# Kernel optimization log

Hardware: AMD Instinct MI355X
Metric: run time of the kernel (lower is better)

The kernel has to match this reference:

```python
import jax, jax.numpy as jnp
import numpy as np

N_NODES = 100000
N_EDGES = 6400000
NODE_IN = 128
HID = 64


def _mlp(x, w1, b1, w2, b2):
    # Linear -> ReLU -> Linear -> ReLU
    return jax.nn.relu(jax.nn.relu(x @ w1 + b1) @ w2 + b2)


def _edge_softmax_agg(node_h, logits, src, dst, n):
    # DGL edge_softmax: softmax of edge logits over incoming edges per dst node,
    # then weighted sum of src node features scattered to dst.
    m = jax.lax.stop_gradient(jax.ops.segment_max(logits, dst, num_segments=n))
    e = jnp.exp(logits - m[dst])
    s = jax.ops.segment_sum(e, dst, num_segments=n)
    w = e / s[dst]
    return jax.ops.segment_sum(w * node_h[src], dst, num_segments=n)


def setup_inputs() -> dict:
    key = jax.random.key(0)
    ks = jax.random.split(key, 24)
    d = {
        "node_feat": jax.random.normal(ks[0], (N_NODES, NODE_IN), jnp.float32),
        "edge_feat": jax.random.normal(ks[1], (N_EDGES, 1), jnp.float32),
        "edge_dist": jax.random.normal(ks[2], (N_EDGES, 1), jnp.float32),
        "src": jax.random.randint(ks[3], (N_EDGES,), 0, N_NODES, jnp.int32),
        "dst": jax.random.randint(ks[4], (N_EDGES,), 0, N_NODES, jnp.int32),
    }
    def lin(k, fin, fout):
        kw, kb = jax.random.split(k)
        return (jax.random.normal(kw, (fin, fout), jnp.float32) / np.sqrt(fin),
                jax.random.normal(kb, (fout,), jnp.float32) * 0.01)
    d["enc_w1"], d["enc_b1"] = lin(ks[5], NODE_IN, HID)
    d["enc_w2"], d["enc_b2"] = lin(ks[6], HID, 1)
    d["nu_w1"], d["nu_b1"] = lin(ks[7], 2, HID)
    d["nu_w2"], d["nu_b2"] = lin(ks[8], HID, 1)
    d["eu_w1"], d["eu_b1"] = lin(ks[9], 3, HID)
    d["eu_w2"], d["eu_b2"] = lin(ks[10], HID, 1)
    d["dec_w1"], d["dec_b1"] = lin(ks[11], 1, HID)
    d["dec_w2"], d["dec_b2"] = lin(ks[12], HID, 1)
    return d


def reference(node_feat, edge_feat, edge_dist, src, dst,
              enc_w1, enc_b1, enc_w2, enc_b2,
              nu_w1, nu_b1, nu_w2, nu_b2,
              eu_w1, eu_b1, eu_w2, eu_b2,
              dec_w1, dec_b1, dec_w2, dec_b2):
    n = node_feat.shape[0]
    # encoder on raw node features -> [N,1]
    h = _mlp(node_feat, enc_w1, enc_b1, enc_w2, enc_b2)
    # softmax aggregation weighted by edge 'dist'
    h = _edge_softmax_agg(h, edge_dist, src, dst, n)
    # edge update: concat([edge_feat, src_h, dst_h]) -> MLP -> [E,1]
    eh = _mlp(jnp.concatenate([edge_feat, h[src], h[dst]], axis=-1),
              eu_w1, eu_b1, eu_w2, eu_b2)
    # pull: sum incoming updated edge features per dst node
    agg = jax.ops.segment_sum(eh, dst, num_segments=n)
    # node update: concat([agg_m, h]) -> MLP -> [N,1]
    h = _mlp(jnp.concatenate([agg, h], axis=-1), nu_w1, nu_b1, nu_w2, nu_b2)
    # second softmax aggregation with updated edge features as logits
    h2 = _edge_softmax_agg(h, eh, src, dst, n)
    # decoder -> [N,1]
    return _mlp(h2, dec_w1, dec_b1, dec_w2, dec_b2)
```

## Files before the change

kernel.cpp:

```cpp
#include <hip/hip_runtime.h>


#define NHB 256

typedef int   iv4 __attribute__((ext_vector_type(4)));
typedef float fv4 __attribute__((ext_vector_type(4)));
typedef float fv2 __attribute__((ext_vector_type(2)));

#if __has_builtin(__builtin_elementwise_fma)
#define FMA2(a, b, c) __builtin_elementwise_fma((a), (b), (c))
#else
static __device__ __forceinline__ fv2 FMA2(fv2 a, fv2 b, fv2 c) {
    fv2 r; r.x = fmaf(a.x, b.x, c.x); r.y = fmaf(a.y, b.y, c.y); return r;
}
#endif
#if __has_builtin(__builtin_elementwise_max)
#define MAX2(a, b) __builtin_elementwise_max((a), (b))
#else
static __device__ __forceinline__ fv2 MAX2(fv2 a, fv2 b) {
    fv2 r; r.x = fmaxf(a.x, b.x); r.y = fmaxf(a.y, b.y); return r;
}
#endif


__global__ void __launch_bounds__(1024) k_chist(
    const int* __restrict__ DST, int* __restrict__ hist,
    int e, int nbkt, int shift, int epb)
{
    __shared__ int lh[512];
    for (int c = threadIdx.x; c < nbkt; c += blockDim.x) lh[c] = 0;
    __syncthreads();
    int b = blockIdx.x;
    int i0 = b * epb, i1 = min(i0 + epb, e);
    int nq = (i1 > i0) ? ((i1 - i0) >> 2) : 0;
    const iv4* D4 = reinterpret_cast<const iv4*>(DST + i0);
    for (int q = threadIdx.x; q < nq; q += blockDim.x) {
        iv4 d = D4[q];
        atomicAdd(&lh[d.x >> shift], 1);
        atomicAdd(&lh[d.y >> shift], 1);
        atomicAdd(&lh[d.z >> shift], 1);
        atomicAdd(&lh[d.w >> shift], 1);
    }
    for (int i = i0 + 4 * nq + threadIdx.x; i < i1; i += blockDim.x)
        atomicAdd(&lh[DST[i] >> shift], 1);
    __syncthreads();
    for (int c = threadIdx.x; c < nbkt; c += blockDim.x)
        hist[(size_t)c * NHB + b] = lh[c];
}

__global__ void __launch_bounds__(256) k_scanA(
    int* __restrict__ hist, int* __restrict__ bktCnt)
{
    int c = blockIdx.x;
    int* row = hist + (size_t)c * NHB;
    __shared__ int part[256];
    int t = threadIdx.x;
    int v = row[t];
    part[t] = v;
    __syncthreads();
    for (int off = 1; off < 256; off <<= 1) {
        int x = 0;
        if (t >= off) x = part[t - off];
        __syncthreads();
        part[t] += x;
        __syncthreads();
    }
    if (t == 255) bktCnt[c] = part[255];
    row[t] = part[t] - v;
}

__global__ void __launch_bounds__(256) k_scanB(
    const int* __restrict__ bktCnt, int* __restrict__ base, int nbkt, int e)
{
    __shared__ int part[256];
    int t = threadIdx.x;
    int v[4];
    int sum = 0;
    #pragma unroll
    for (int u = 0; u < 4; ++u) {
        int idx = t * 4 + u;
        v[u] = (idx < nbkt) ? bktCnt[idx] : 0;
        sum += v[u];
    }
    part[t] = sum;
    __syncthreads();
    for (int off = 1; off < 256; off <<= 1) {
        int x = 0;
        if (t >= off) x = part[t - off];
        __syncthreads();
        part[t] += x;
        __syncthreads();
    }
    int run = (t == 0) ? 0 : part[t - 1];
    #pragma unroll
    for (int u = 0; u < 4; ++u) {
        int idx = t * 4 + u;
        if (idx < nbkt) base[idx] = run;
        run += v[u];
    }
    if (t == 0) base[nbkt] = e;
}

__global__ void __launch_bounds__(1024) k_scatter(
    const int* __restrict__ DST, const int* __restrict__ SRC,
    const float* __restrict__ DIST, const float* __restrict__ EF,
    const int* __restrict__ hist, const int* __restrict__ base,
    float2* __restrict__ payA, float* __restrict__ ef_s,
    int e, int nbkt, int shift, int epb)
{
    __shared__ int loff[512];
    int b = blockIdx.x;
    for (int c = threadIdx.x; c < nbkt; c += blockDim.x)
        loff[c] = base[c] + hist[(size_t)c * NHB + b];
    __syncthreads();
    int i0 = b * epb, i1 = min(i0 + epb, e);
    if (i0 >= i1) return;
    int mask = (1 << shift) - 1;
    int nq = (i1 - i0) >> 2;
    const iv4* D4 = reinterpret_cast<const iv4*>(DST + i0);
    const iv4* S4 = reinterpret_cast<const iv4*>(SRC + i0);
    const fv4* T4 = reinterpret_cast<const fv4*>(DIST + i0);
    const fv4* F4 = reinterpret_cast<const fv4*>(EF + i0);
    for (int q = threadIdx.x; q < nq; q += blockDim.x) {
        iv4 dv = __builtin_nontemporal_load(D4 + q);
        iv4 sv = __builtin_nontemporal_load(S4 + q);
        fv4 tv = __builtin_nontemporal_load(T4 + q);
        fv4 fv = __builtin_nontemporal_load(F4 + q);
        #pragma unroll
        for (int u = 0; u < 4; ++u) {
            int d = dv[u];
            int c = d >> shift;
            int pos = atomicAdd(&loff[c], 1);
            int sd = (sv[u] << shift) | (d & mask);
            payA[pos] = make_float2(__int_as_float(sd), tv[u]);
            ef_s[pos] = fv[u];
        }
    }
    for (int i = i0 + 4 * nq + threadIdx.x; i < i1; i += blockDim.x) {
        int d = DST[i];
        int c = d >> shift;
        int pos = atomicAdd(&loff[c], 1);
        int sd = (SRC[i] << shift) | (d & mask);
        payA[pos] = make_float2(__int_as_float(sd), DIST[i]);
        ef_s[pos] = EF[i];
    }
}


__global__ void __launch_bounds__(256) k_enc(
    const float* __restrict__ X, const float* __restrict__ W1,
    const float* __restrict__ B1, const float* __restrict__ W2,
    const float* __restrict__ B2, float* __restrict__ H0, int n)
{
    __shared__ float4 w1s[2048];
    for (int t = threadIdx.x; t < 2048; t += blockDim.x)
        w1s[t] = reinterpret_cast<const float4*>(W1)[t];
    __syncthreads();

    int i = blockIdx.x * blockDim.x + threadIdx.x;
    if (i >= n) return;

    const float4* xp = reinterpret_cast<const float4*>(X) + (size_t)i * 32;

    float acc[64];
    #pragma unroll
    for (int j = 0; j < 64; ++j) acc[j] = B1[j];

    for (int k4 = 0; k4 < 32; ++k4) {
        float4 xv = xp[k4];
        #pragma unroll
        for (int kk = 0; kk < 4; ++kk) {
            float x = (&xv.x)[kk];
            const float4* wrow = &w1s[(k4 * 4 + kk) * 16];
            #pragma unroll
            for (int j4 = 0; j4 < 16; ++j4) {
                float4 w = wrow[j4];
                acc[j4*4+0] = fmaf(x, w.x, acc[j4*4+0]);
                acc[j4*4+1] = fmaf(x, w.y, acc[j4*4+1]);
                acc[j4*4+2] = fmaf(x, w.z, acc[j4*4+2]);
                acc[j4*4+3] = fmaf(x, w.w, acc[j4*4+3]);
            }
        }
    }
    float o = B2[0];
    #pragma unroll
    for (int j = 0; j < 64; ++j)
        o = fmaf(fmaxf(acc[j], 0.f), W2[j], o);
    H0[i] = fmaxf(o, 0.f);
}


__global__ void __launch_bounds__(256) k_passA(
    const float2* __restrict__ payA, const float* __restrict__ H0,
    const int* __restrict__ base,
    float* __restrict__ pSum, float* __restrict__ pNum, int shift, int G)
{
    __shared__ float lsum[512], lnum[512];
    int c = blockIdx.x / G, g = blockIdx.x % G;
    int bw = 1 << shift, mask = bw - 1;
    for (int t = threadIdx.x; t < bw; t += blockDim.x) { lsum[t] = 0.f; lnum[t] = 0.f; }
    __syncthreads();
    int b0 = base[c], len = base[c + 1] - b0;
    int i0 = b0 + (int)(((long long)len * g) / G);
    int i1 = b0 + (int)(((long long)len * (g + 1)) / G);
    const int T = blockDim.x;
    for (int i = i0 + (int)threadIdx.x; i < i1; i += 2 * T) {
        int jb = i + T;
        fv2 p0 = __builtin_nontemporal_load(
            reinterpret_cast<const fv2*>(payA) + i);
        fv2 p1 = {0.f, 0.f};
        bool vb = jb < i1;
        if (vb) p1 = __builtin_nontemporal_load(
                    reinterpret_cast<const fv2*>(payA) + jb);
        int sd0 = __float_as_int(p0.x);
        int sd1 = __float_as_int(p1.x);
        float h0a = H0[sd0 >> shift];
        float h0b = vb ? H0[sd1 >> shift] : 0.f;
        float e0 = __expf(p0.y);
        float e1 = __expf(p1.y);
        atomicAdd(&lsum[sd0 & mask], e0);
        atomicAdd(&lnum[sd0 & mask], e0 * h0a);
        if (vb) {
            atomicAdd(&lsum[sd1 & mask], e1);
            atomicAdd(&lnum[sd1 & mask], e1 * h0b);
        }
    }
    __syncthreads();
    size_t po = (size_t)blockIdx.x << shift;
    for (int t = threadIdx.x; t < bw; t += blockDim.x) {
        pSum[po + t] = lsum[t];
        pNum[po + t] = lnum[t];
    }
}

__global__ void __launch_bounds__(256) k_finA(
    const float* __restrict__ pSum, const float* __restrict__ pNum,
    float* __restrict__ H1, int shift, int n, int G)
{
    int d = blockIdx.x * blockDim.x + threadIdx.x;
    if (d >= n) return;
    int c = d >> shift, t = d & ((1 << shift) - 1);
    size_t b = (size_t)c * G << shift;
    int bw = 1 << shift;
    float s = 0.f, m = 0.f;
    for (int g = 0; g < G; ++g) {
        s += pSum[b + (size_t)g * bw + t];
        m += pNum[b + (size_t)g * bw + t];
    }
    H1[d] = (s != 0.f) ? m / s : 0.f;
}

__global__ void __launch_bounds__(256) k_passB(
    const float2* __restrict__ payA, float* __restrict__ ef_s,
    const float* __restrict__ H1,
    const float* __restrict__ W1, const float* __restrict__ B1,
    const float* __restrict__ W2, const float* __restrict__ B2,
    const int* __restrict__ base,
    float* __restrict__ pAgg, float* __restrict__ pS2, int shift, int n, int G)
{
    __shared__ float h1loc[512], lagg[512], ls2[512];
    const fv2 ZERO2 = {0.f, 0.f};
    int bw = 1 << shift, mask = bw - 1;
    int c = blockIdx.x / G, g = blockIdx.x % G;
    int d0 = c << shift;
    for (int t = threadIdx.x; t < bw; t += blockDim.x) {
        int d = d0 + t;
        h1loc[t] = (d < n) ? H1[d] : 0.f;
        lagg[t] = 0.f;
        ls2[t] = 0.f;
    }
    __syncthreads();
    const float b2 = B2[0];
    int b0 = base[c], len = base[c + 1] - b0;
    int i0 = b0 + (int)(((long long)len * g) / G);
    int i1 = b0 + (int)(((long long)len * (g + 1)) / G);
    const int T = blockDim.x;

    int i = i0 + (int)threadIdx.x;
    fv2 pa[4]; float xf[4];
    #pragma unroll
    for (int u = 0; u < 4; ++u) {
        int j = i + u * T;
        pa[u] = ZERO2; xf[u] = 0.f;
        if (j < i1) {
            pa[u] = __builtin_nontemporal_load(
                reinterpret_cast<const fv2*>(payA) + j);
            xf[u] = __builtin_nontemporal_load(ef_s + j);
        }
    }
    while (i < i1) {
        int inext = i + 4 * T;
        fv2 pb[4]; float xg[4];
        #pragma unroll
        for (int u = 0; u < 4; ++u) {
            int j = inext + u * T;
            pb[u] = ZERO2; xg[u] = 0.f;
            if (j < i1) {
                pb[u] = __builtin_nontemporal_load(
                    reinterpret_cast<const fv2*>(payA) + j);
                xg[u] = __builtin_nontemporal_load(ef_s + j);
            }
        }
        fv2 x0v[4], hsv[4], hdv[4], o2[4];
        int lo[4];
        #pragma unroll
        for (int u = 0; u < 4; ++u) {
            int sd = __float_as_int(pa[u].x);
            lo[u] = sd & mask;
            float hs = H1[sd >> shift];
            float hd = h1loc[lo[u]];
            fv2 xt; xt.x = xf[u]; xt.y = xf[u];
            x0v[u] = xt;
            fv2 ht; ht.x = hs; ht.y = hs;
            hsv[u] = ht;
            fv2 dt; dt.x = hd; dt.y = hd;
            hdv[u] = dt;
            o2[u] = ZERO2;
        }
        #pragma unroll 4
        for (int j = 0; j < 64; j += 2) {
            fv2 aj = *reinterpret_cast<const fv2*>(W1 + j);
            fv2 bj = *reinterpret_cast<const fv2*>(W1 + 64 + j);
            fv2 cj = *reinterpret_cast<const fv2*>(W1 + 128 + j);
            fv2 dj = *reinterpret_cast<const fv2*>(B1 + j);
            fv2 vj = *reinterpret_cast<const fv2*>(W2 + j);
            #pragma unroll
            for (int u = 0; u < 4; ++u) {
                fv2 t = FMA2(x0v[u], aj,
                         FMA2(hsv[u], bj, FMA2(hdv[u], cj, dj)));
                t = MAX2(t, ZERO2);
                o2[u] = FMA2(t, vj, o2[u]);
            }
        }
        #pragma unroll
        for (int u = 0; u < 4; ++u) {
            int j = i + u * T;
            if (j < i1) {
                float eh = fmaxf(o2[u].x + o2[u].y + b2, 0.f);
                float ex = __expf(eh);
                ef_s[j] = ex;
                atomicAdd(&lagg[lo[u]], eh);
                atomicAdd(&ls2[lo[u]], ex);
            }
        }
        i = inext;
        #pragma unroll
        for (int u = 0; u < 4; ++u) { pa[u] = pb[u]; xf[u] = xg[u]; }
    }
    __syncthreads();
    size_t po = (size_t)blockIdx.x << shift;
    for (int t = threadIdx.x; t < bw; t += blockDim.x) {
        pAgg[po + t] = lagg[t];
        pS2[po + t] = ls2[t];
    }
}

__global__ void __launch_bounds__(256) k_finB(
    const float* __restrict__ pAgg, const float* __restrict__ pS2,
    const float* __restrict__ H1,
    const float* __restrict__ NW1, const float* __restrict__ NB1,
    const float* __restrict__ NW2, const float* __restrict__ NB2,
    float* __restrict__ H2, float* __restrict__ S2, int shift, int n, int G)
{
    int d = blockIdx.x * blockDim.x + threadIdx.x;
    if (d >= n) return;
    int c = d >> shift, t = d & ((1 << shift) - 1);
    size_t b = (size_t)c * G << shift;
    int bw = 1 << shift;
    float agg = 0.f, s2 = 0.f;
    for (int g = 0; g < G; ++g) {
        agg += pAgg[b + (size_t)g * bw + t];
        s2  += pS2[b + (size_t)g * bw + t];
    }
    float xh = H1[d];
    float o = NB2[0];
    #pragma unroll 4
    for (int j = 0; j < 64; ++j) {
        float a = fmaf(agg, NW1[j], fmaf(xh, NW1[64 + j], NB1[j]));
        o = fmaf(fmaxf(a, 0.f), NW2[j], o);
    }
    H2[d] = fmaxf(o, 0.f);
    S2[d] = s2;
}

__global__ void __launch_bounds__(256) k_passC(
    const float2* __restrict__ payA, const float* __restrict__ e2_s,
    const float* __restrict__ H2, const int* __restrict__ base,
    float* __restrict__ pNum, int shift, int G)
{
    __shared__ float lnum[512];
    int c = blockIdx.x / G, g = blockIdx.x % G;
    int bw = 1 << shift, mask = bw - 1;
    for (int t = threadIdx.x; t < bw; t += blockDim.x) lnum[t] = 0.f;
    __syncthreads();
    int b0 = base[c], len = base[c + 1] - b0;
    int i0 = b0 + (int)(((long long)len * g) / G);
    int i1 = b0 + (int)(((long long)len * (g + 1)) / G);
    const int T = blockDim.x;
    for (int i = i0 + (int)threadIdx.x; i < i1; i += 2 * T) {
        int jb = i + T;
        bool vb = jb < i1;
        fv2 p0 = __builtin_nontemporal_load(
            reinterpret_cast<const fv2*>(payA) + i);
        float e0 = __builtin_nontemporal_load(e2_s + i);
        fv2 p1 = {0.f, 0.f};
        float e1 = 0.f;
        if (vb) {
            p1 = __builtin_nontemporal_load(
                reinterpret_cast<const fv2*>(payA) + jb);
            e1 = __builtin_nontemporal_load(e2_s + jb);
        }
        int sd0 = __float_as_int(p0.x);
        int sd1 = __float_as_int(p1.x);
        float m0 = e0 * H2[sd0 >> shift];
        float m1 = vb ? e1 * H2[sd1 >> shift] : 0.f;
        atomicAdd(&lnum[sd0 & mask], m0);
        if (vb) atomicAdd(&lnum[sd1 & mask], m1);
    }
    __syncthreads();
    size_t po = (size_t)blockIdx.x << shift;
    for (int t = threadIdx.x; t < bw; t += blockDim.x)
        pNum[po + t] = lnum[t];
}

__global__ void __launch_bounds__(256) k_finC(
    const float* __restrict__ pNum, const float* __restrict__ S2,
    const float* __restrict__ W1, const float* __restrict__ B1,
    const float* __restrict__ W2, const float* __restrict__ B2,
    float* __restrict__ OUT, int shift, int n, int G)
{
    int d = blockIdx.x * blockDim.x + threadIdx.x;
    if (d >= n) return;
    int c = d >> shift, t = d & ((1 << shift) - 1);
    size_t b = (size_t)c * G << shift;
    int bw = 1 << shift;
    float m = 0.f;
    for (int g = 0; g < G; ++g) m += pNum[b + (size_t)g * bw + t];
    float s = S2[d];
    float x = (s != 0.f) ? m / s : 0.f;
    float o = B2[0];
    #pragma unroll 4
    for (int j = 0; j < 64; ++j) {
        float a = fmaf(x, W1[j], B1[j]);
        o = fmaf(fmaxf(a, 0.f), W2[j], o);
    }
    OUT[d] = fmaxf(o, 0.f);
}


__device__ __forceinline__ void atomAddF(float* p, float v) { unsafeAtomicAdd(p, v); }

__global__ void k_zero(float* __restrict__ p, int n) {
    int i = blockIdx.x * blockDim.x + threadIdx.x;
    if (i < n) p[i] = 0.f;
}

__global__ void __launch_bounds__(256) k_agg1(
    const float* __restrict__ DIST, const int* __restrict__ SRC,
    const int* __restrict__ DST, const float* __restrict__ H0,
    float* __restrict__ S1, float* __restrict__ NUM1, int e)
{
    int i = blockIdx.x * blockDim.x + threadIdx.x;
    if (i >= e) return;
    float ev = __expf(DIST[i]);
    atomAddF(&S1[DST[i]], ev);
    atomAddF(&NUM1[DST[i]], ev * H0[SRC[i]]);
}

__global__ void k_div(const float* __restrict__ NUM, const float* __restrict__ S,
                      float* __restrict__ H, int n) {
    int i = blockIdx.x * blockDim.x + threadIdx.x;
    if (i < n) {
        float s = S[i];
        H[i] = (s != 0.f) ? NUM[i] / s : 0.f;
    }
}

__global__ void __launch_bounds__(256) k_edgeF(
    const float* __restrict__ EF, const int* __restrict__ SRC,
    const int* __restrict__ DST, const float* __restrict__ H1,
    const float* __restrict__ W1, const float* __restrict__ B1,
    const float* __restrict__ W2, const float* __restrict__ B2,
    float* __restrict__ E2, float* __restrict__ AGG, float* __restrict__ S2, int e)
{
    int i = blockIdx.x * blockDim.x + threadIdx.x;
    if (i >= e) return;
    float x0 = EF[i];
    int s = SRC[i], d = DST[i];
    float h_s = H1[s], h_d = H1[d];
    float o = B2[0];
    for (int j = 0; j < 64; ++j) {
        float aj = fmaf(x0, W1[j], fmaf(h_s, W1[64+j], fmaf(h_d, W1[128+j], B1[j])));
        o = fmaf(fmaxf(aj, 0.f), W2[j], o);
    }
    float eh = fmaxf(o, 0.f);
    float ex = __expf(eh);
    E2[i] = ex;
    atomAddF(&AGG[d], eh);
    atomAddF(&S2[d], ex);
}

__global__ void k_nu(const float* __restrict__ AGG, const float* __restrict__ H1,
                     const float* __restrict__ W1, const float* __restrict__ B1,
                     const float* __restrict__ W2, const float* __restrict__ B2,
                     float* __restrict__ H2, int n)
{
    int i = blockIdx.x * blockDim.x + threadIdx.x;
    if (i >= n) return;
    float x0 = AGG[i], x1 = H1[i];
    float o = B2[0];
    #pragma unroll
    for (int j = 0; j < 64; ++j) {
        float a = fmaf(x0, W1[j], fmaf(x1, W1[64 + j], B1[j]));
        o = fmaf(fmaxf(a, 0.f), W2[j], o);
    }
    H2[i] = fmaxf(o, 0.f);
}

__global__ void __launch_bounds__(256) k_agg2F(
    const float* __restrict__ E2, const int* __restrict__ SRC,
    const int* __restrict__ DST, const float* __restrict__ H2,
    float* __restrict__ NUM2, int e)
{
    int i = blockIdx.x * blockDim.x + threadIdx.x;
    if (i >= e) return;
    atomAddF(&NUM2[DST[i]], E2[i] * H2[SRC[i]]);
}

__global__ void k_final(const float* __restrict__ NUM2, const float* __restrict__ S2,
                        const float* __restrict__ W1, const float* __restrict__ B1,
                        const float* __restrict__ W2, const float* __restrict__ B2,
                        float* __restrict__ OUT, int n)
{
    int i = blockIdx.x * blockDim.x + threadIdx.x;
    if (i >= n) return;
    float s = S2[i];
    float x = (s != 0.f) ? NUM2[i] / s : 0.f;
    float o = B2[0];
    #pragma unroll
    for (int j = 0; j < 64; ++j) {
        float a = fmaf(x, W1[j], B1[j]);
        o = fmaf(fmaxf(a, 0.f), W2[j], o);
    }
    OUT[i] = fmaxf(o, 0.f);
}


extern "C" void kernel_launch(void* const* d_in, const int* in_sizes, int n_in,
                              void* d_out, int out_size, void* d_ws, size_t ws_size,
                              hipStream_t stream)
{
    const float* node_feat = (const float*)d_in[0];
    const float* edge_feat = (const float*)d_in[1];
    const float* edge_dist = (const float*)d_in[2];
    const int*   src       = (const int*)d_in[3];
    const int*   dst       = (const int*)d_in[4];
    const float* enc_w1 = (const float*)d_in[5];
    const float* enc_b1 = (const float*)d_in[6];
    const float* enc_w2 = (const float*)d_in[7];
    const float* enc_b2 = (const float*)d_in[8];
    const float* nu_w1  = (const float*)d_in[9];
    const float* nu_b1  = (const float*)d_in[10];
    const float* nu_w2  = (const float*)d_in[11];
    const float* nu_b2  = (const float*)d_in[12];
    const float* eu_w1  = (const float*)d_in[13];
    const float* eu_b1  = (const float*)d_in[14];
    const float* eu_w2  = (const float*)d_in[15];
    const float* eu_b2  = (const float*)d_in[16];
    const float* dec_w1 = (const float*)d_in[17];
    const float* dec_b1 = (const float*)d_in[18];
    const float* dec_w2 = (const float*)d_in[19];
    const float* dec_b2 = (const float*)d_in[20];

    const int n = in_sizes[0] / 128;
    const int e = in_sizes[1];
    const int B = 256;

    int shift = 9;
    while ((((n + (1 << shift) - 1) >> shift) > 512) && shift < 12) shift++;
    const int nbkt = (n + (1 << shift) - 1) >> shift;
    int epb = (e + NHB - 1) / NHB;
    epb = (epb + 3) & ~3;

    float* ws = (float*)d_ws;
    size_t w = (size_t)4 * n;
    int* base   = (int*)(ws + w); w += nbkt + 1;
    int* bktCnt = (int*)(ws + w); w += nbkt;
    int* hist   = (int*)(ws + w); w += (size_t)nbkt * NHB;
    w = (w + 1) & ~(size_t)1;
    float2* payA = (float2*)(ws + w); w += (size_t)2 * e;
    float* ef_s  = ws + w; w += e;

    int G = 16;
    size_t psz;
    size_t need;
    for (;;) {
        psz = ((size_t)nbkt * G) << shift;
        need = (w + 2 * psz) * 4;
        if (need <= ws_size || G == 1) break;
        G >>= 1;
    }
    float* pP0 = ws + w;
    float* pP1 = ws + w + psz;

    float* h0 = ws;
    float* h1 = ws + (size_t)1 * n;
    float* h2 = ws + (size_t)2 * n;
    float* s2 = ws + (size_t)3 * n;

    if (ws_size >= need && nbkt <= 512 && (1 << shift) <= 512 &&
        ((size_t)n << shift) < (1u << 30)) {
        const int gE = nbkt * G;
        hipLaunchKernelGGL(k_chist, dim3(NHB), dim3(1024), 0, stream,
                           dst, hist, e, nbkt, shift, epb);
        hipLaunchKernelGGL(k_scanA, dim3(nbkt), dim3(B), 0, stream, hist, bktCnt);
        hipLaunchKernelGGL(k_scanB, dim3(1), dim3(B), 0, stream, bktCnt, base, nbkt, e);
        hipLaunchKernelGGL(k_scatter, dim3(NHB), dim3(1024), 0, stream,
                           dst, src, edge_dist, edge_feat, hist, base,
                           payA, ef_s, e, nbkt, shift, epb);
        hipLaunchKernelGGL(k_enc, dim3((n + B - 1) / B), dim3(B), 0, stream,
                           node_feat, enc_w1, enc_b1, enc_w2, enc_b2, h0, n);
        hipLaunchKernelGGL(k_passA, dim3(gE), dim3(B), 0, stream,
                           payA, h0, base, pP0, pP1, shift, G);
        hipLaunchKernelGGL(k_finA, dim3((n + B - 1) / B), dim3(B), 0, stream,
                           pP0, pP1, h1, shift, n, G);
        hipLaunchKernelGGL(k_passB, dim3(gE), dim3(B), 0, stream,
                           payA, ef_s, h1, eu_w1, eu_b1, eu_w2, eu_b2, base,
                           pP0, pP1, shift, n, G);
        hipLaunchKernelGGL(k_finB, dim3((n + B - 1) / B), dim3(B), 0, stream,
                           pP0, pP1, h1, nu_w1, nu_b1, nu_w2, nu_b2, h2, s2,
                           shift, n, G);
        hipLaunchKernelGGL(k_passC, dim3(gE), dim3(B), 0, stream,
                           payA, ef_s , h2, base, pP0, shift, G);
        hipLaunchKernelGGL(k_finC, dim3((n + B - 1) / B), dim3(B), 0, stream,
                           pP0, s2, dec_w1, dec_b1, dec_w2, dec_b2,
                           (float*)d_out, shift, n, G);
    } else {
        float* agg  = ws + (size_t)2 * n;
        float* s1   = ws + (size_t)4 * n;
        float* num1 = ws + (size_t)5 * n;
        float* num2 = ws + (size_t)6 * n;
        float* h2f  = ws + (size_t)7 * n;
        float* e2   = ws + (size_t)8 * n;
        hipLaunchKernelGGL(k_zero, dim3((5 * n + B - 1) / B), dim3(B), 0, stream,
                           agg, 5 * n);
        hipLaunchKernelGGL(k_enc, dim3((n + B - 1) / B), dim3(B), 0, stream,
                           node_feat, enc_w1, enc_b1, enc_w2, enc_b2, h0, n);
        hipLaunchKernelGGL(k_agg1, dim3((e + B - 1) / B), dim3(B), 0, stream,
                           edge_dist, src, dst, h0, s1, num1, e);
        hipLaunchKernelGGL(k_div, dim3((n + B - 1) / B), dim3(B), 0, stream,
                           num1, s1, h1, n);
        hipLaunchKernelGGL(k_edgeF, dim3((e + B - 1) / B), dim3(B), 0, stream,
                           edge_feat, src, dst, h1, eu_w1, eu_b1, eu_w2, eu_b2,
                           e2, agg, s2, e);
        hipLaunchKernelGGL(k_nu, dim3((n + B - 1) / B), dim3(B), 0, stream,
                           agg, h1, nu_w1, nu_b1, nu_w2, nu_b2, h2f, n);
        hipLaunchKernelGGL(k_agg2F, dim3((e + B - 1) / B), dim3(B), 0, stream,
                           e2, src, dst, h2f, num2, e);
        hipLaunchKernelGGL(k_final, dim3((n + B - 1) / B), dim3(B), 0, stream,
                           num2, s2, dec_w1, dec_b1, dec_w2, dec_b2, (float*)d_out, n);
    }
}
```

Before: 385.8 us.

## Deepen edge-MLP prefetch to 8 edges and compute per-edge MLP sequentially

The edge-update kernel now prefetches 8 edges per thread per iteration instead of 4, and gathers all 8 source-node H1 values up front. The 64-wide hidden-layer MLP is moved inside the per-edge loop, so each edge runs its own MLP rather than four edges being interleaved per weight load. This aims to hide more gather latency, but it reloads the weights once per edge instead of amortising each load across four edges, and it raises register pressure from the larger prefetch buffers.

```diff
diff --git a/kernel.cpp b/kernel.cpp
--- a/kernel.cpp
+++ b/kernel.cpp
@@ -277,9 +277,9 @@
     const int T = blockDim.x;
 
     int i = i0 + (int)threadIdx.x;
-    fv2 pa[4]; float xf[4];
+    fv2 pa[8]; float xf[8];
     #pragma unroll
-    for (int u = 0; u < 4; ++u) {
+    for (int u = 0; u < 8; ++u) {
         int j = i + u * T;
         pa[u] = ZERO2; xf[u] = 0.f;
         if (j < i1) {
@@ -289,10 +289,10 @@
         }
     }
     while (i < i1) {
-        int inext = i + 4 * T;
-        fv2 pb[4]; float xg[4];
+        int inext = i + 8 * T;
+        fv2 pb[8]; float xg[8];
         #pragma unroll
-        for (int u = 0; u < 4; ++u) {
+        for (int u = 0; u < 8; ++u) {
             int j = inext + u * T;
             pb[u] = ZERO2; xg[u] = 0.f;
             if (j < i1) {
@@ -301,42 +301,34 @@
                 xg[u] = __builtin_nontemporal_load(ef_s + j);
             }
         }
-        fv2 x0v[4], hsv[4], hdv[4], o2[4];
-        int lo[4];
+        float hs[8]; int lo[8];
         #pragma unroll
-        for (int u = 0; u < 4; ++u) {
+        for (int u = 0; u < 8; ++u) {
             int sd = __float_as_int(pa[u].x);
             lo[u] = sd & mask;
-            float hs = H1[sd >> shift];
-            float hd = h1loc[lo[u]];
-            fv2 xt; xt.x = xf[u]; xt.y = xf[u];
-            x0v[u] = xt;
-            fv2 ht; ht.x = hs; ht.y = hs;
-            hsv[u] = ht;
-            fv2 dt; dt.x = hd; dt.y = hd;
-            hdv[u] = dt;
-            o2[u] = ZERO2;
-        }
-        #pragma unroll 4
-        for (int j = 0; j < 64; j += 2) {
-            fv2 aj = *reinterpret_cast<const fv2*>(W1 + j);
-            fv2 bj = *reinterpret_cast<const fv2*>(W1 + 64 + j);
-            fv2 cj = *reinterpret_cast<const fv2*>(W1 + 128 + j);
-            fv2 dj = *reinterpret_cast<const fv2*>(B1 + j);
-            fv2 vj = *reinterpret_cast<const fv2*>(W2 + j);
-            #pragma unroll
-            for (int u = 0; u < 4; ++u) {
-                fv2 t = FMA2(x0v[u], aj,
-                         FMA2(hsv[u], bj, FMA2(hdv[u], cj, dj)));
-                t = MAX2(t, ZERO2);
-                o2[u] = FMA2(t, vj, o2[u]);
-            }
+            hs[u] = H1[sd >> shift];
         }
         #pragma unroll
-        for (int u = 0; u < 4; ++u) {
+        for (int u = 0; u < 8; ++u) {
             int j = i + u * T;
             if (j < i1) {
-                float eh = fmaxf(o2[u].x + o2[u].y + b2, 0.f);
+                float hd = h1loc[lo[u]];
+                fv2 xv; xv.x = xf[u]; xv.y = xf[u];
+                fv2 hv; hv.x = hs[u]; hv.y = hs[u];
+                fv2 dv; dv.x = hd;    dv.y = hd;
+                fv2 o2 = ZERO2;
+                #pragma unroll 8
+                for (int jj = 0; jj < 64; jj += 2) {
+                    fv2 aj = *reinterpret_cast<const fv2*>(W1 + jj);
+                    fv2 bj = *reinterpret_cast<const fv2*>(W1 + 64 + jj);
+                    fv2 cj = *reinterpret_cast<const fv2*>(W1 + 128 + jj);
+                    fv2 dj = *reinterpret_cast<const fv2*>(B1 + jj);
+                    fv2 vj = *reinterpret_cast<const fv2*>(W2 + jj);
+                    fv2 t = FMA2(xv, aj, FMA2(hv, bj, FMA2(dv, cj, dj)));
+                    t = MAX2(t, ZERO2);
+                    o2 = FMA2(t, vj, o2);
+                }
+                float eh = fmaxf(o2.x + o2.y + b2, 0.f);
                 float ex = __expf(eh);
                 ef_s[j] = ex;
                 atomicAdd(&lagg[lo[u]], eh);
@@ -345,7 +337,7 @@
         }
         i = inext;
         #pragma unroll
-        for (int u = 0; u < 4; ++u) { pa[u] = pb[u]; xf[u] = xg[u]; }
+        for (int u = 0; u < 8; ++u) { pa[u] = pb[u]; xf[u] = xg[u]; }
     }
     __syncthreads();
     size_t po = (size_t)blockIdx.x << shift;
```

Result: no change. 386.9 us (+0.3%).
